# Kernel tuning notes

Measured on AMD Instinct MI355X. Metric: run time of the kernel, lower is better.

The kernel has to match this reference:

```python
import jax, jax.numpy as jnp
import numpy as np

B, N, D, S, ITERS = 64, 4096, 256, 8, 3
EPS = 1e-5


def _ln(x, g, b):
    m = jnp.mean(x, axis=-1, keepdims=True)
    v = jnp.mean((x - m) ** 2, axis=-1, keepdims=True)
    return (x - m) * jax.lax.rsqrt(v + EPS) * g + b


def setup_inputs() -> dict:
    key = jax.random.key(0)
    ks = jax.random.split(key, 20)
    s = 1.0 / np.sqrt(D)
    inp = {
        'x': jax.random.normal(ks[0], (B, N, D), jnp.float32),
        'noise': jax.random.normal(ks[1], (B, S, D), jnp.float32),
        'slot_mu': jax.random.normal(ks[2], (1, 1, D), jnp.float32),
        'slot_sigma': jax.random.normal(ks[3], (1, 1, D), jnp.float32) * 0.1,
        'Wq': jax.random.uniform(ks[4], (D, D), jnp.float32, -s, s),
        'bq': jnp.zeros((D,), jnp.float32),
        'Wk': jax.random.uniform(ks[5], (D, D), jnp.float32, -s, s),
        'bk': jnp.zeros((D,), jnp.float32),
        'Wv': jax.random.uniform(ks[6], (D, D), jnp.float32, -s, s),
        'bv': jnp.zeros((D,), jnp.float32),
        'W_ih': jax.random.uniform(ks[7], (3 * D, D), jnp.float32, -s, s),
        'b_ih': jnp.zeros((3 * D,), jnp.float32),
        'W_hh': jax.random.uniform(ks[8], (3 * D, D), jnp.float32, -s, s),
        'b_hh': jnp.zeros((3 * D,), jnp.float32),
        'W1': jax.random.uniform(ks[9], (D, D), jnp.float32, -s, s),
        'b1': jnp.zeros((D,), jnp.float32),
        'W2': jax.random.uniform(ks[10], (D, D), jnp.float32, -s, s),
        'b2': jnp.zeros((D,), jnp.float32),
        'g_in': jnp.ones((D,), jnp.float32), 'be_in': jnp.zeros((D,), jnp.float32),
        'g_sl': jnp.ones((D,), jnp.float32), 'be_sl': jnp.zeros((D,), jnp.float32),
        'g_mlp': jnp.ones((D,), jnp.float32), 'be_mlp': jnp.zeros((D,), jnp.float32),
    }
    return inp


def reference(x, noise, slot_mu, slot_sigma, Wq, bq, Wk, bk, Wv, bv,
              W_ih, b_ih, W_hh, b_hh, W1, b1, W2, b2,
              g_in, be_in, g_sl, be_sl, g_mlp, be_mlp):
    # slot init: mu + exp(sigma) * noise, broadcast over (B, S, D)
    slots = slot_mu + jnp.exp(slot_sigma) * noise

    xn = _ln(x, g_in, be_in)
    k = jnp.einsum('bnd,ed->bne', xn, Wk) + bk
    v = jnp.einsum('bnd,ed->bne', xn, Wv) + bv

    for _ in range(ITERS):
        sn = _ln(slots, g_sl, be_sl)
        q = jnp.einsum('bsd,ed->bse', sn, Wq) + bq
        attn_logits = jnp.einsum('bsd,bnd->bsn', q, k)
        attn = jax.nn.softmax(attn_logits, axis=-1)  # softmax over inputs N (as in source)
        updates = jnp.einsum('bnd,bsn->bsd', v, attn)

        # GRUCell: input=updates, hidden=slots (flattened over B*S)
        u = updates.reshape(-1, D)
        h = slots.reshape(-1, D)
        gx = u @ W_ih.T + b_ih
        gh = h @ W_hh.T + b_hh
        xr, xz, xn_g = jnp.split(gx, 3, axis=-1)
        hr, hz, hn_g = jnp.split(gh, 3, axis=-1)
        r = jax.nn.sigmoid(xr + hr)
        z = jax.nn.sigmoid(xz + hz)
        n = jnp.tanh(xn_g + r * hn_g)
        h = (1.0 - z) * n + z * h
        slots = h.reshape(x.shape[0], -1, D)

        m = _ln(slots, g_mlp, be_mlp)
        slots = slots + jax.nn.relu(m @ W1.T + b1) @ W2.T + b2
    return slots
```

## Files before the change

kernel.cpp:

```cpp
#include <hip/hip_runtime.h>

#define B_ 64
#define N_ 4096
#define D_ 256
#define S_ 8
#define EPSL 1e-5f

typedef _Float16 f16x8 __attribute__((ext_vector_type(8)));
typedef _Float16 f16x4 __attribute__((ext_vector_type(4)));
typedef float f32x4 __attribute__((ext_vector_type(4)));

__device__ __forceinline__ void gload_lds16(const void* g, void* l){
    __builtin_amdgcn_global_load_lds(
        (const __attribute__((address_space(1))) unsigned int*)g,
        (__attribute__((address_space(3))) unsigned int*)l, 16, 0, 0);
}

__device__ __forceinline__ void a16_st4(_Float16* a, int row, int col, float4 v){
    int byte = row*512 + ((col*2) ^ ((row&7)<<4));
    f16x4 h; h[0]=(_Float16)v.x; h[1]=(_Float16)v.y; h[2]=(_Float16)v.z; h[3]=(_Float16)v.w;
    *(f16x4*)((char*)a + byte) = h;
}
__device__ __forceinline__ void a16_st2(_Float16* a, int row, int col, _Float16 v){
    int byte = row*512 + ((col*2) ^ ((row&7)<<4));
    *(_Float16*)((char*)a + byte) = v;
}
__device__ __forceinline__ f16x8 a16_ld8(const _Float16* a, int row, int col){
    int byte = row*512 + ((col*2) ^ ((row&7)<<4));
    return *(const f16x8*)((const char*)a + byte);
}
__device__ __forceinline__ f16x8 wfrag_ld(const _Float16* __restrict__ Wf,
        int tt, int ks, int l){
    return *(const f16x8*)(Wf + ((long)tt*4096 + (ks*64 + l)*8));
}

__global__ __launch_bounds__(256) void k_ln_x(const float* __restrict__ x,
        const float* __restrict__ g, const float* __restrict__ be,
        _Float16* __restrict__ xn) {
    int w = threadIdx.x >> 6, l = threadIdx.x & 63;
    long row = (long)blockIdx.x * 4 + w;
    float4 xv = *(const float4*)(x + row * D_ + l * 4);
    float s = xv.x + xv.y + xv.z + xv.w;
    float q = xv.x*xv.x + xv.y*xv.y + xv.z*xv.z + xv.w*xv.w;
    #pragma unroll
    for (int m = 1; m < 64; m <<= 1) { s += __shfl_xor(s, m); q += __shfl_xor(q, m); }
    float mean = s * (1.0f/D_);
    float var = q * (1.0f/D_) - mean*mean;
    float inv = rsqrtf(var + EPSL);
    float4 gv = *(const float4*)(g + l*4);
    float4 bv = *(const float4*)(be + l*4);
    f16x4 o;
    o[0] = (_Float16)((xv.x-mean)*inv*gv.x + bv.x);
    o[1] = (_Float16)((xv.y-mean)*inv*gv.y + bv.y);
    o[2] = (_Float16)((xv.z-mean)*inv*gv.z + bv.z);
    o[3] = (_Float16)((xv.w-mean)*inv*gv.w + bv.w);
    *(f16x4*)(xn + row * D_ + l*4) = o;
}

__global__ __launch_bounds__(256) void k_wpre(const float* __restrict__ Whh,
        const float* __restrict__ W1, const float* __restrict__ W2,
        _Float16* __restrict__ Whhf, _Float16* __restrict__ W1f,
        _Float16* __restrict__ W2f,
        const float* __restrict__ Wih, const float* __restrict__ Wv,
        const float* __restrict__ Wq, const float* __restrict__ Wk,
        const float* __restrict__ bih, const float* __restrict__ bv,
        const float* __restrict__ bq, _Float16* __restrict__ Wcf,
        _Float16* __restrict__ Wqkf, float* __restrict__ bc,
        float* __restrict__ cq) {
    __shared__ float a4[4][256];
    int r = blockIdx.x, t = threadIdx.x;
    int w = t>>6, l = t&63;
    if (r >= 256){
        int rr = r - 256;
        const float* src; _Float16* dst; int row;
        if (rr < 768){ src = Whh; dst = Whhf; row = rr; }
        else if (rr < 1024){ src = W1; dst = W1f; row = rr - 768; }
        else { src = W2; dst = W2f; row = rr - 1024; }
        float v = src[(long)row*256 + t];
        long di = (long)((((row>>4)*8 + (t>>5))*64 + ((t>>3)&3)*16 + (row&15)))*8 + (t&7);
        dst[di] = (_Float16)v;
        return;
    }
    bool isC = (r < 192);
    if (isC){
        #pragma unroll
        for (int k=0;k<4;k++) a4[k][t] = Wih[(long)(r*4+k)*256 + t];
    } else {
        int dbase = (r-192)*4;
        #pragma unroll
        for (int k=0;k<4;k++) a4[k][t] = Wk[(long)t*256 + dbase + k];
    }
    __syncthreads();
    float ac[4] = {0.f,0.f,0.f,0.f};
    const float* Bm = isC ? Wv : Wq;
    for (int e=0;e<256;e++){
        float bvv = Bm[(long)e*256 + t];
        ac[0] += a4[0][e]*bvv; ac[1] += a4[1][e]*bvv;
        ac[2] += a4[2][e]*bvv; ac[3] += a4[3][e]*bvv;
    }
    _Float16* dst = isC ? Wcf : Wqkf;
    int rb = isC ? r*4 : (r-192)*4;
    #pragma unroll
    for (int k=0;k<4;k++){
        int row = rb + k;
        long di = (long)((((row>>4)*8 + (t>>5))*64 + ((t>>3)&3)*16 + (row&15)))*8 + (t&7);
        dst[di] = (_Float16)ac[k];
    }
    if (w < 4){
        const float* bvec = isC ? bv : bq;
        float p = 0.f;
        #pragma unroll
        for (int q=0;q<4;q++) p += a4[w][l + q*64] * bvec[l + q*64];
        #pragma unroll
        for (int m=1;m<64;m<<=1) p += __shfl_xor(p, m);
        if (l==0){
            if (isC) bc[r*4 + w] = p + bih[r*4 + w];
            else     cq[(r-192)*4 + w] = p;
        }
    }
}

template<int NT, int OS>
__device__ __forceinline__ void mm_stage_f(const _Float16* a16,
        const _Float16* __restrict__ Wf, float* outl, int w, int l){
    int lr = l&15, lh = l>>4;
    f16x8 A[8];
    #pragma unroll
    for (int ks=0;ks<8;ks++) A[ks] = a16_ld8(a16, lr, lh*8 + ks*32);
    #pragma unroll
    for (int tile=0; tile<NT; ++tile){
        int tt = w*NT + tile;
        f32x4 acc = {0.f,0.f,0.f,0.f};
        #pragma unroll
        for (int ks=0;ks<8;ks++)
            acc = __builtin_amdgcn_mfma_f32_16x16x32_f16(A[ks], wfrag_ld(Wf,tt,ks,l), acc, 0,0,0);
        if (lh < 2){
            #pragma unroll
            for (int r=0;r<4;r++) outl[(lh*4+r)*OS + tt*16 + lr] = acc[r];
        }
    }
}

__device__ __forceinline__ void mm_gates_f(const _Float16* au, const _Float16* ah,
        const _Float16* __restrict__ Wcf, const _Float16* __restrict__ Whf,
        float* g1, float* g2, int w, int l){
    int lr = l&15, lh = l>>4;
    f16x8 Au[8], Ah[8];
    #pragma unroll
    for (int ks=0;ks<8;ks++){ Au[ks] = a16_ld8(au, lr, lh*8+ks*32);
                              Ah[ks] = a16_ld8(ah, lr, lh*8+ks*32); }
    #pragma unroll
    for (int tile=0; tile<6; ++tile){
        int tt = w*6 + tile;
        f32x4 a1 = {0.f,0.f,0.f,0.f}, a2 = {0.f,0.f,0.f,0.f};
        #pragma unroll
        for (int ks=0;ks<8;ks++)
            a1 = __builtin_amdgcn_mfma_f32_16x16x32_f16(Au[ks], wfrag_ld(Wcf,tt,ks,l), a1, 0,0,0);
        #pragma unroll
        for (int ks=0;ks<8;ks++)
            a2 = __builtin_amdgcn_mfma_f32_16x16x32_f16(Ah[ks], wfrag_ld(Whf,tt,ks,l), a2, 0,0,0);
        if (lh < 2){
            #pragma unroll
            for (int r=0;r<4;r++){
                int s = lh*4+r;
                g1[s*768 + tt*16 + lr] = a1[r];
                g2[s*768 + tt*16 + lr] = a2[r];
            }
        }
    }
}

__global__ __launch_bounds__(512) void k_init(const float* __restrict__ noise,
        const float* __restrict__ mu, const float* __restrict__ sg,
        const float* __restrict__ g_sl, const float* __restrict__ be_sl,
        const _Float16* __restrict__ Wqkf, const float* __restrict__ cq,
        float* __restrict__ slots, _Float16* __restrict__ qh16) {
    __shared__ __align__(16) _Float16 a16[16*256];
    __shared__ float g1[8*256];
    int t = threadIdx.x, w = t>>6, l = t&63, b = blockIdx.x;
    int col = l*4;
    float4 nz = *(const float4*)(noise + ((long)b*8+w)*256 + col);
    float4 muv = *(const float4*)(mu + col);
    float4 sgv = *(const float4*)(sg + col);
    float4 sl;
    sl.x = muv.x + __expf(sgv.x)*nz.x; sl.y = muv.y + __expf(sgv.y)*nz.y;
    sl.z = muv.z + __expf(sgv.z)*nz.z; sl.w = muv.w + __expf(sgv.w)*nz.w;
    *(float4*)(slots + ((long)b*8+w)*256 + col) = sl;
    float s1 = sl.x+sl.y+sl.z+sl.w;
    float s2 = sl.x*sl.x+sl.y*sl.y+sl.z*sl.z+sl.w*sl.w;
    #pragma unroll
    for (int m=1;m<64;m<<=1){ s1+=__shfl_xor(s1,m); s2+=__shfl_xor(s2,m); }
    float mean = s1*(1.0f/D_);
    float inv = rsqrtf(s2*(1.0f/D_) - mean*mean + EPSL);
    float4 gv = *(const float4*)(g_sl + col);
    float4 bb = *(const float4*)(be_sl + col);
    float4 sn;
    sn.x=(sl.x-mean)*inv*gv.x+bb.x; sn.y=(sl.y-mean)*inv*gv.y+bb.y;
    sn.z=(sl.z-mean)*inv*gv.z+bb.z; sn.w=(sl.w-mean)*inv*gv.w+bb.w;
    a16_st4(a16, w, col, sn);
    float4 z = {0.f,0.f,0.f,0.f};
    a16_st4(a16, 8+w, col, z);
    __syncthreads();
    mm_stage_f<2,256>(a16, Wqkf, g1, w, l);
    __syncthreads();
    for (int idx=t; idx<2048; idx+=512){
        int s = idx>>8, d = idx&255;
        qh16[((long)b*16+s)*D_ + d] = (_Float16)(g1[s*256+d] + cq[d]);
        qh16[((long)b*16+8+s)*D_ + d] = (_Float16)0.f;
    }
}

__global__ __launch_bounds__(256) void k_attn(const _Float16* __restrict__ xn,
        const _Float16* __restrict__ qh16,
        _Float16* __restrict__ pacc, float* __restrict__ ppsum,
        float* __restrict__ pmax) {
    __shared__ __align__(16) char xt_raw[4*16384];
    __shared__ __align__(16) float pt_s[4][16][8];
    __shared__ float mw_s[4][8], psw_s[4][8];
    int t = threadIdx.x, w = t>>6, l = t&63, lr = l&15, lh = l>>4;
    int c = blockIdx.x, b = blockIdx.y;

    f16x8 A[8];
    const _Float16* qbase = qh16 + ((long)b*16 + lr)*D_ + lh*8;
    #pragma unroll
    for (int ks=0;ks<8;ks++) A[ks] = *(const f16x8*)(qbase + ks*32);
    asm volatile("s_waitcnt vmcnt(0)" ::: "memory");

    char* xw = xt_raw + w*16384;
    const char* xnb = (const char*)(xn + (long)b*N_*D_);
    int rlo = l>>5;
    int cb  = (l&31)*16;

    {   int n0 = c*512 + w*16;
        #pragma unroll
        for (int j=0;j<8;j++){
            int row = 2*j + rlo;
            const char* gp = xnb + (long)(n0+row)*512 + (cb ^ ((row&7)<<4));
            gload_lds16(gp, xw + j*1024);
        }
    }

    float m8[8];
    #pragma unroll
    for (int s=0;s<8;s++) m8[s] = -1e30f;
    float acc[8][4] = {};
    float psr[4] = {0.f,0.f,0.f,0.f};
    float (*pt)[8] = pt_s[w];
    int fx = (lr&7)<<4;

    for (int sc=0; sc<8; ++sc){
        const char* curb = xw + ((sc&1)<<13);
        char* nxtb = xw + (((sc+1)&1)<<13);
        if (sc < 7){
            asm volatile("s_waitcnt lgkmcnt(0)" ::: "memory");
            int n0n = c*512 + (sc+1)*64 + w*16;
            #pragma unroll
            for (int j=0;j<8;j++){
                int row = 2*j + rlo;
                const char* gp = xnb + (long)(n0n+row)*512 + (cb ^ ((row&7)<<4));
                gload_lds16(gp, nxtb + j*1024);
            }
            asm volatile("s_waitcnt vmcnt(8)" ::: "memory");
        } else {
            asm volatile("s_waitcnt vmcnt(0)" ::: "memory");
        }
        __builtin_amdgcn_sched_barrier(0);

        f32x4 lacc = {0.f,0.f,0.f,0.f};
        #pragma unroll
        for (int ks=0;ks<8;ks++){
            f16x8 Bf = *(const f16x8*)(curb + lr*512 + ((lh*16 + ks*64) ^ fx));
            lacc = __builtin_amdgcn_mfma_f32_16x16x32_f16(A[ks], Bf, lacc, 0,0,0);
        }
        float tm[4];
        #pragma unroll
        for (int r=0;r<4;r++) tm[r] = lacc[r];
        #pragma unroll
        for (int m=1;m<16;m<<=1){
            #pragma unroll
            for (int r=0;r<4;r++) tm[r] = fmaxf(tm[r], __shfl_xor(tm[r], m));
        }
        float mN[8];
        #pragma unroll
        for (int r=0;r<4;r++){ mN[r] = __shfl(tm[r], lr); mN[4+r] = __shfl(tm[r], 16+lr); }
        float sc8[8];
        #pragma unroll
        for (int s=0;s<8;s++){
            float mn = fmaxf(m8[s], mN[s]);
            sc8[s] = __expf(m8[s] - mn);
            m8[s] = mn;
        }
        #pragma unroll
        for (int s=0;s<8;s++){
            acc[s][0]*=sc8[s]; acc[s][1]*=sc8[s]; acc[s][2]*=sc8[s]; acc[s][3]*=sc8[s];
        }
        if (lh < 2){
            float4 pv;
            #pragma unroll
            for (int r=0;r<4;r++){
                int s = lh*4+r;
                float p = __expf(lacc[r] - m8[s]);
                psr[r] = psr[r]*sc8[s] + p;
                ((float*)&pv)[r] = p;
            }
            *(float4*)&pt[lr][lh*4] = pv;
        }
        #pragma unroll 4
        for (int i=0;i<16;i++){
            float4 p0 = *(const float4*)&pt[i][0];
            float4 p1 = *(const float4*)&pt[i][4];
            f16x4 xv = *(const f16x4*)(curb + i*512 + ((l*8) ^ ((i&7)<<4)));
            float x0=(float)xv[0], x1=(float)xv[1], x2=(float)xv[2], x3=(float)xv[3];
            acc[0][0]+=p0.x*x0; acc[0][1]+=p0.x*x1; acc[0][2]+=p0.x*x2; acc[0][3]+=p0.x*x3;
            acc[1][0]+=p0.y*x0; acc[1][1]+=p0.y*x1; acc[1][2]+=p0.y*x2; acc[1][3]+=p0.y*x3;
            acc[2][0]+=p0.z*x0; acc[2][1]+=p0.z*x1; acc[2][2]+=p0.z*x2; acc[2][3]+=p0.z*x3;
            acc[3][0]+=p0.w*x0; acc[3][1]+=p0.w*x1; acc[3][2]+=p0.w*x2; acc[3][3]+=p0.w*x3;
            acc[4][0]+=p1.x*x0; acc[4][1]+=p1.x*x1; acc[4][2]+=p1.x*x2; acc[4][3]+=p1.x*x3;
            acc[5][0]+=p1.y*x0; acc[5][1]+=p1.y*x1; acc[5][2]+=p1.y*x2; acc[5][3]+=p1.y*x3;
            acc[6][0]+=p1.z*x0; acc[6][1]+=p1.z*x1; acc[6][2]+=p1.z*x2; acc[6][3]+=p1.z*x3;
            acc[7][0]+=p1.w*x0; acc[7][1]+=p1.w*x1; acc[7][2]+=p1.w*x2; acc[7][3]+=p1.w*x3;
        }
    }
    #pragma unroll
    for (int m=1;m<16;m<<=1){
        #pragma unroll
        for (int r=0;r<4;r++) psr[r] += __shfl_xor(psr[r], m);
    }
    if (l == 0){
        #pragma unroll
        for (int s=0;s<8;s++) mw_s[w][s] = m8[s];
        #pragma unroll
        for (int r=0;r<4;r++) psw_s[w][r] = psr[r];
    }
    if (l == 16){
        #pragma unroll
        for (int r=0;r<4;r++) psw_s[w][4+r] = psr[r];
    }
    __syncthreads();
    float M8[8];
    #pragma unroll
    for (int s=0;s<8;s++)
        M8[s] = fmaxf(fmaxf(mw_s[0][s],mw_s[1][s]), fmaxf(mw_s[2][s],mw_s[3][s]));
    float* accw = (float*)xt_raw;
    #pragma unroll
    for (int s=0;s<8;s++){
        float wsc = __expf(m8[s] - M8[s]);
        float4 v;
        v.x=acc[s][0]*wsc; v.y=acc[s][1]*wsc; v.z=acc[s][2]*wsc; v.w=acc[s][3]*wsc;
        *(float4*)&accw[((w*8+s)<<8) + l*4] = v;
    }
    __syncthreads();
    for (int pair=t; pair<2048; pair+=256){
        int s = pair>>8, d = pair&255;
        float v = accw[(s<<8)+d] + accw[((8+s)<<8)+d] + accw[((16+s)<<8)+d] + accw[((24+s)<<8)+d];
        pacc[(((long)b*8 + c)*8 + s)*D_ + d] = (_Float16)v;
    }
    if (t < 8){
        float ps = 0.f;
        #pragma unroll
        for (int w2=0;w2<4;w2++) ps += __expf(mw_s[w2][t]-M8[t]) * psw_s[w2][t];
        ppsum[((long)b*8+c)*8 + t] = ps;
        pmax [((long)b*8+c)*8 + t] = M8[t];
    }
}

__global__ __launch_bounds__(512) void k_tail(
    const _Float16* __restrict__ pacc, const float* __restrict__ ppsum,
    const float* __restrict__ pmax, const float* __restrict__ slots,
    const _Float16* __restrict__ Wcf, const float* __restrict__ bc,
    const _Float16* __restrict__ Whhf, const float* __restrict__ bhh,
    const _Float16* __restrict__ W1f, const float* __restrict__ b1,
    const _Float16* __restrict__ W2f, const float* __restrict__ b2,
    const float* __restrict__ gm, const float* __restrict__ bem,
    const float* __restrict__ g_sl, const float* __restrict__ be_sl,
    const _Float16* __restrict__ Wqkf, const float* __restrict__ cq,
    float* __restrict__ out, _Float16* __restrict__ qh16, int last) {
    int t = threadIdx.x, w = t>>6, l = t&63;
    int b = blockIdx.x;
    __shared__ float hb[8][256], hn[8][256];
    __shared__ float g1[8*768], g2[8*768];
    __shared__ __align__(16) _Float16 a16a[16*256], a16b[16*256];
    __shared__ float pss[8];
    __shared__ float wcs[8][8];

    if (t < 8){
        float pm[8]; float M = -1e30f;
        #pragma unroll
        for (int c=0;c<8;c++){ pm[c] = pmax[((long)b*8+c)*8+t]; M = fmaxf(M, pm[c]); }
        float ps = 0.f;
        #pragma unroll
        for (int c=0;c<8;c++){
            float wc = __expf(pm[c]-M);
            wcs[t][c] = wc;
            ps += wc*ppsum[((long)b*8+c)*8+t];
        }
        pss[t] = ps;
    }
    __syncthreads();
    for (int idx=t; idx<2048; idx+=512){
        int s = idx>>8, d = idx&255;
        float v = 0.f;
        #pragma unroll
        for (int c=0;c<8;c++) v += wcs[s][c]*(float)pacc[(((long)b*8+c)*8+s)*D_ + d];
        float axv = v / pss[s];
        float hbv = slots[((long)b*8+s)*D_ + d];
        hb[s][d] = hbv;
        a16_st2(a16a, s, d, (_Float16)axv);
        a16_st2(a16b, s, d, (_Float16)hbv);
    }
    {   float4 z = {0.f,0.f,0.f,0.f};
        a16_st4(a16a, 8+w, l*4, z);
        a16_st4(a16b, 8+w, l*4, z);
    }
    __syncthreads();
    mm_gates_f(a16a, a16b, Wcf, Whhf, g1, g2, w, l);
    __syncthreads();
    {
        int d0 = l*4;
        float hn4[4];
        #pragma unroll
        for (int i=0;i<4;i++){
            int d = d0+i;
            float r = 1.f/(1.f+__expf(-(g1[w*768+d]     + bc[d]     + g2[w*768+d]     + bhh[d])));
            float z = 1.f/(1.f+__expf(-(g1[w*768+256+d] + bc[256+d] + g2[w*768+256+d] + bhh[256+d])));
            float gg = g1[w*768+512+d] + bc[512+d] + r*(g2[w*768+512+d] + bhh[512+d]);
            float e2 = __expf(2.f*gg);
            float nn = 1.f - 2.f/(e2+1.f);
            hn4[i] = (1.f-z)*nn + z*hb[w][d];
            hn[w][d] = hn4[i];
        }
        float s1 = hn4[0]+hn4[1]+hn4[2]+hn4[3];
        float s2 = hn4[0]*hn4[0]+hn4[1]*hn4[1]+hn4[2]*hn4[2]+hn4[3]*hn4[3];
        #pragma unroll
        for (int m=1;m<64;m<<=1){ s1+=__shfl_xor(s1,m); s2+=__shfl_xor(s2,m); }
        float mean = s1*(1.0f/D_);
        float inv = rsqrtf(s2*(1.0f/D_) - mean*mean + EPSL);
        float4 gv = *(const float4*)(gm + d0);
        float4 bb = *(const float4*)(bem + d0);
        float4 v;
        v.x=(hn4[0]-mean)*inv*gv.x+bb.x; v.y=(hn4[1]-mean)*inv*gv.y+bb.y;
        v.z=(hn4[2]-mean)*inv*gv.z+bb.z; v.w=(hn4[3]-mean)*inv*gv.w+bb.w;
        a16_st4(a16a, w, d0, v);
    }
    __syncthreads();
    mm_stage_f<2,256>(a16a, W1f, g1, w, l);
    __syncthreads();
    {
        int d0 = l*4;
        float4 v = *(const float4*)&g1[w*256+d0];
        float4 bb = *(const float4*)(b1 + d0);
        v.x=fmaxf(v.x+bb.x,0.f); v.y=fmaxf(v.y+bb.y,0.f);
        v.z=fmaxf(v.z+bb.z,0.f); v.w=fmaxf(v.w+bb.w,0.f);
        a16_st4(a16b, w, d0, v);
    }
    __syncthreads();
    mm_stage_f<2,256>(a16b, W2f, g2, w, l);
    __syncthreads();
    {
        int d0 = l*4;
        float4 bb = *(const float4*)(b2 + d0);
        float4 o4;
        o4.x = hn[w][d0]   + g2[w*256+d0]   + bb.x;
        o4.y = hn[w][d0+1] + g2[w*256+d0+1] + bb.y;
        o4.z = hn[w][d0+2] + g2[w*256+d0+2] + bb.z;
        o4.w = hn[w][d0+3] + g2[w*256+d0+3] + bb.w;
        *(float4*)(out + ((long)b*8+w)*D_ + d0) = o4;
        if (!last){
            float s1 = o4.x+o4.y+o4.z+o4.w;
            float s2 = o4.x*o4.x+o4.y*o4.y+o4.z*o4.z+o4.w*o4.w;
            #pragma unroll
            for (int m=1;m<64;m<<=1){ s1+=__shfl_xor(s1,m); s2+=__shfl_xor(s2,m); }
            float mean = s1*(1.0f/D_);
            float inv = rsqrtf(s2*(1.0f/D_) - mean*mean + EPSL);
            float4 gv = *(const float4*)(g_sl + d0);
            float4 be = *(const float4*)(be_sl + d0);
            float4 v;
            v.x=(o4.x-mean)*inv*gv.x+be.x; v.y=(o4.y-mean)*inv*gv.y+be.y;
            v.z=(o4.z-mean)*inv*gv.z+be.z; v.w=(o4.w-mean)*inv*gv.w+be.w;
            a16_st4(a16a, w, d0, v);
        }
    }
    if (last) return;
    __syncthreads();
    mm_stage_f<2,256>(a16a, Wqkf, g1, w, l);
    __syncthreads();
    for (int idx=t; idx<2048; idx+=512){
        int s = idx>>8, d = idx&255;
        qh16[((long)b*16+s)*D_ + d] = (_Float16)(g1[s*256+d] + cq[d]);
    }
}

extern "C" void kernel_launch(void* const* d_in, const int* in_sizes, int n_in,
                              void* d_out, int out_size, void* d_ws, size_t ws_size,
                              hipStream_t stream) {
    const float* x     = (const float*)d_in[0];
    const float* noise = (const float*)d_in[1];
    const float* mu    = (const float*)d_in[2];
    const float* sg    = (const float*)d_in[3];
    const float* Wq    = (const float*)d_in[4];
    const float* bq    = (const float*)d_in[5];
    const float* Wk    = (const float*)d_in[6];
    const float* Wv    = (const float*)d_in[8];
    const float* bv    = (const float*)d_in[9];
    const float* Wih   = (const float*)d_in[10];
    const float* bih   = (const float*)d_in[11];
    const float* Whh   = (const float*)d_in[12];
    const float* bhh   = (const float*)d_in[13];
    const float* W1    = (const float*)d_in[14];
    const float* b1    = (const float*)d_in[15];
    const float* W2    = (const float*)d_in[16];
    const float* b2    = (const float*)d_in[17];
    const float* g_in  = (const float*)d_in[18];
    const float* be_in = (const float*)d_in[19];
    const float* g_sl  = (const float*)d_in[20];
    const float* be_sl = (const float*)d_in[21];
    const float* g_mlp = (const float*)d_in[22];
    const float* be_mlp= (const float*)d_in[23];

    char* ws = (char*)d_ws;
    _Float16* xn16  = (_Float16*)(ws);
    _Float16* qh16  = (_Float16*)(ws + 134217728);
    float*    slots = (float*)   (ws + 134742016);
    _Float16* pacc  = (_Float16*)(ws + 135266304);
    float*    ppsum = (float*)   (ws + 152043520);
    float*    pmax  = (float*)   (ws + 152059904);
    _Float16* w16f  = (_Float16*)(ws + 152076288);
    float*    bc    = (float*)   (ws + 153255936);
    float*    cq    = (float*)   (ws + 153259008);

    _Float16* Wcf  = w16f;
    _Float16* Whhf = w16f + 196608;
    _Float16* W1f  = w16f + 393216;
    _Float16* W2f  = w16f + 458752;
    _Float16* Wqkf = w16f + 524288;

    hipLaunchKernelGGL(k_wpre, dim3(1536), dim3(256), 0, stream,
                       Whh, W1, W2, Whhf, W1f, W2f,
                       Wih, Wv, Wq, Wk, bih, bv, bq, Wcf, Wqkf, bc, cq);
    hipLaunchKernelGGL(k_ln_x, dim3(65536), dim3(256), 0, stream, x, g_in, be_in, xn16);
    hipLaunchKernelGGL(k_init, dim3(64), dim3(512), 0, stream,
                       noise, mu, sg, g_sl, be_sl, Wqkf, cq, slots, qh16);
    for (int it = 0; it < 3; it++){
        hipLaunchKernelGGL(k_attn, dim3(8,64), dim3(256), 0, stream,
                           xn16, qh16, pacc, ppsum, pmax);
        float* dst = (it==2) ? (float*)d_out : slots;
        hipLaunchKernelGGL(k_tail, dim3(64), dim3(512), 0, stream,
                           pacc, ppsum, pmax, slots,
                           Wcf, bc, Whhf, bhh, W1f, b1, W2f, b2,
                           g_mlp, be_mlp, g_sl, be_sl, Wqkf, cq,
                           dst, qh16, (it==2) ? 1 : 0);
    }
}
```

Before: 269.0 us.

## Fuse input LayerNorm into first attention pass and use nontemporal LDS loads

Removes the standalone LayerNorm kernel over x and computes the normalization inside a new first-iteration attention kernel. That kernel normalizes fp32 rows, writes the fp16 result to LDS for immediate use, and also stores it to global memory for later iterations. This avoids one full write-then-read pass of the normalized activations in the first iteration. The fused kernel loses the async double-buffered prefetch and exposes register-heavy fp32 loads. The later attention kernels now use a nontemporal cache hint on their global-to-LDS loads.

```diff
diff --git a/kernel.cpp b/kernel.cpp
--- a/kernel.cpp
+++ b/kernel.cpp
@@ -10,10 +10,10 @@
 typedef _Float16 f16x4 __attribute__((ext_vector_type(4)));
 typedef float f32x4 __attribute__((ext_vector_type(4)));
 
-__device__ __forceinline__ void gload_lds16(const void* g, void* l){
+__device__ __forceinline__ void gload_lds16_nt(const void* g, void* l){
     __builtin_amdgcn_global_load_lds(
         (const __attribute__((address_space(1))) unsigned int*)g,
-        (__attribute__((address_space(3))) unsigned int*)l, 16, 0, 0);
+        (__attribute__((address_space(3))) unsigned int*)l, 16, 0, 2);
 }
 
 __device__ __forceinline__ void a16_st4(_Float16* a, int row, int col, float4 v){
@@ -32,29 +32,6 @@
 __device__ __forceinline__ f16x8 wfrag_ld(const _Float16* __restrict__ Wf,
         int tt, int ks, int l){
     return *(const f16x8*)(Wf + ((long)tt*4096 + (ks*64 + l)*8));
-}
-
-__global__ __launch_bounds__(256) void k_ln_x(const float* __restrict__ x,
-        const float* __restrict__ g, const float* __restrict__ be,
-        _Float16* __restrict__ xn) {
-    int w = threadIdx.x >> 6, l = threadIdx.x & 63;
-    long row = (long)blockIdx.x * 4 + w;
-    float4 xv = *(const float4*)(x + row * D_ + l * 4);
-    float s = xv.x + xv.y + xv.z + xv.w;
-    float q = xv.x*xv.x + xv.y*xv.y + xv.z*xv.z + xv.w*xv.w;
-    #pragma unroll
-    for (int m = 1; m < 64; m <<= 1) { s += __shfl_xor(s, m); q += __shfl_xor(q, m); }
-    float mean = s * (1.0f/D_);
-    float var = q * (1.0f/D_) - mean*mean;
-    float inv = rsqrtf(var + EPSL);
-    float4 gv = *(const float4*)(g + l*4);
-    float4 bv = *(const float4*)(be + l*4);
-    f16x4 o;
-    o[0] = (_Float16)((xv.x-mean)*inv*gv.x + bv.x);
-    o[1] = (_Float16)((xv.y-mean)*inv*gv.y + bv.y);
-    o[2] = (_Float16)((xv.z-mean)*inv*gv.z + bv.z);
-    o[3] = (_Float16)((xv.w-mean)*inv*gv.w + bv.w);
-    *(f16x4*)(xn + row * D_ + l*4) = o;
 }
 
 __global__ __launch_bounds__(256) void k_wpre(const float* __restrict__ Whh,
@@ -210,6 +187,170 @@
     }
 }
 
+__global__ __launch_bounds__(256) void k_attn1(const float* __restrict__ x,
+        const float* __restrict__ g_in, const float* __restrict__ be_in,
+        _Float16* __restrict__ xn,
+        const _Float16* __restrict__ qh16,
+        _Float16* __restrict__ pacc, float* __restrict__ ppsum,
+        float* __restrict__ pmax) {
+    __shared__ __align__(16) char xt_raw[4*16384];
+    __shared__ __align__(16) float pt_s[4][16][8];
+    __shared__ float mw_s[4][8], psw_s[4][8];
+    int t = threadIdx.x, w = t>>6, l = t&63, lr = l&15, lh = l>>4;
+    int c = blockIdx.x, b = blockIdx.y;
+
+    f16x8 A[8];
+    const _Float16* qbase = qh16 + ((long)b*16 + lr)*D_ + lh*8;
+    #pragma unroll
+    for (int ks=0;ks<8;ks++) A[ks] = *(const f16x8*)(qbase + ks*32);
+
+    char* xw = xt_raw + w*16384;
+    int rq = l>>2, q = l&3;
+
+    float m8[8];
+    #pragma unroll
+    for (int s=0;s<8;s++) m8[s] = -1e30f;
+    float acc[8][4] = {};
+    float psr[4] = {0.f,0.f,0.f,0.f};
+    float (*pt)[8] = pt_s[w];
+    int fx = (lr&7)<<4;
+
+    for (int sc=0; sc<8; ++sc){
+        char* curb = xw + ((sc&1)<<13);
+        int n0 = c*512 + sc*64 + w*16;
+        const float* xf = x + ((long)(b*N_) + n0 + rq)*D_ + q*64;
+        float4 xv[16];
+        #pragma unroll
+        for (int i=0;i<16;i++) xv[i] = *(const float4*)(xf + i*4);
+        float s1 = 0.f, s2 = 0.f;
+        #pragma unroll
+        for (int i=0;i<16;i++){
+            s1 += xv[i].x + xv[i].y + xv[i].z + xv[i].w;
+            s2 += xv[i].x*xv[i].x + xv[i].y*xv[i].y + xv[i].z*xv[i].z + xv[i].w*xv[i].w;
+        }
+        s1 += __shfl_xor(s1, 1); s2 += __shfl_xor(s2, 1);
+        s1 += __shfl_xor(s1, 2); s2 += __shfl_xor(s2, 2);
+        float mean = s1 * (1.0f/D_);
+        float inv = rsqrtf(s2 * (1.0f/D_) - mean*mean + EPSL);
+        int swz = (rq&7)<<4;
+        _Float16* gout = xn + ((long)(b*N_) + n0 + rq)*D_ + q*64;
+        #pragma unroll
+        for (int k=0;k<8;k++){
+            float4 v0 = xv[k*2], v1 = xv[k*2+1];
+            float4 gv0 = *(const float4*)(g_in + q*64 + k*8);
+            float4 gv1 = *(const float4*)(g_in + q*64 + k*8 + 4);
+            float4 bb0 = *(const float4*)(be_in + q*64 + k*8);
+            float4 bb1 = *(const float4*)(be_in + q*64 + k*8 + 4);
+            f16x8 o;
+            o[0]=(_Float16)((v0.x-mean)*inv*gv0.x+bb0.x);
+            o[1]=(_Float16)((v0.y-mean)*inv*gv0.y+bb0.y);
+            o[2]=(_Float16)((v0.z-mean)*inv*gv0.z+bb0.z);
+            o[3]=(_Float16)((v0.w-mean)*inv*gv0.w+bb0.w);
+            o[4]=(_Float16)((v1.x-mean)*inv*gv1.x+bb1.x);
+            o[5]=(_Float16)((v1.y-mean)*inv*gv1.y+bb1.y);
+            o[6]=(_Float16)((v1.z-mean)*inv*gv1.z+bb1.z);
+            o[7]=(_Float16)((v1.w-mean)*inv*gv1.w+bb1.w);
+            *(f16x8*)(curb + rq*512 + ((q*128 + k*16) ^ swz)) = o;
+            *(f16x8*)(gout + k*8) = o;
+        }
+        f32x4 lacc = {0.f,0.f,0.f,0.f};
+        #pragma unroll
+        for (int ks=0;ks<8;ks++){
+            f16x8 Bf = *(const f16x8*)(curb + lr*512 + ((lh*16 + ks*64) ^ fx));
+            lacc = __builtin_amdgcn_mfma_f32_16x16x32_f16(A[ks], Bf, lacc, 0,0,0);
+        }
+        float tm[4];
+        #pragma unroll
+        for (int r=0;r<4;r++) tm[r] = lacc[r];
+        #pragma unroll
+        for (int m=1;m<16;m<<=1){
+            #pragma unroll
+            for (int r=0;r<4;r++) tm[r] = fmaxf(tm[r], __shfl_xor(tm[r], m));
+        }
+        float mN[8];
+        #pragma unroll
+        for (int r=0;r<4;r++){ mN[r] = __shfl(tm[r], lr); mN[4+r] = __shfl(tm[r], 16+lr); }
+        float sc8[8];
+        #pragma unroll
+        for (int s=0;s<8;s++){
+            float mn = fmaxf(m8[s], mN[s]);
+            sc8[s] = __expf(m8[s] - mn);
+            m8[s] = mn;
+        }
+        #pragma unroll
+        for (int s=0;s<8;s++){
+            acc[s][0]*=sc8[s]; acc[s][1]*=sc8[s]; acc[s][2]*=sc8[s]; acc[s][3]*=sc8[s];
+        }
+        if (lh < 2){
+            float4 pv;
+            #pragma unroll
+            for (int r=0;r<4;r++){
+                int s = lh*4+r;
+                float p = __expf(lacc[r] - m8[s]);
+                psr[r] = psr[r]*sc8[s] + p;
+                ((float*)&pv)[r] = p;
+            }
+            *(float4*)&pt[lr][lh*4] = pv;
+        }
+        #pragma unroll 4
+        for (int i=0;i<16;i++){
+            float4 p0 = *(const float4*)&pt[i][0];
+            float4 p1 = *(const float4*)&pt[i][4];
+            f16x4 xvv = *(const f16x4*)(curb + i*512 + ((l*8) ^ ((i&7)<<4)));
+            float x0=(float)xvv[0], x1=(float)xvv[1], x2=(float)xvv[2], x3=(float)xvv[3];
+            acc[0][0]+=p0.x*x0; acc[0][1]+=p0.x*x1; acc[0][2]+=p0.x*x2; acc[0][3]+=p0.x*x3;
+            acc[1][0]+=p0.y*x0; acc[1][1]+=p0.y*x1; acc[1][2]+=p0.y*x2; acc[1][3]+=p0.y*x3;
+            acc[2][0]+=p0.z*x0; acc[2][1]+=p0.z*x1; acc[2][2]+=p0.z*x2; acc[2][3]+=p0.z*x3;
+            acc[3][0]+=p0.w*x0; acc[3][1]+=p0.w*x1; acc[3][2]+=p0.w*x2; acc[3][3]+=p0.w*x3;
+            acc[4][0]+=p1.x*x0; acc[4][1]+=p1.x*x1; acc[4][2]+=p1.x*x2; acc[4][3]+=p1.x*x3;
+            acc[5][0]+=p1.y*x0; acc[5][1]+=p1.y*x1; acc[5][2]+=p1.y*x2; acc[5][3]+=p1.y*x3;
+            acc[6][0]+=p1.z*x0; acc[6][1]+=p1.z*x1; acc[6][2]+=p1.z*x2; acc[6][3]+=p1.z*x3;
+            acc[7][0]+=p1.w*x0; acc[7][1]+=p1.w*x1; acc[7][2]+=p1.w*x2; acc[7][3]+=p1.w*x3;
+        }
+    }
+    #pragma unroll
+    for (int m=1;m<16;m<<=1){
+        #pragma unroll
+        for (int r=0;r<4;r++) psr[r] += __shfl_xor(psr[r], m);
+    }
+    if (l == 0){
+        #pragma unroll
+        for (int s=0;s<8;s++) mw_s[w][s] = m8[s];
+        #pragma unroll
+        for (int r=0;r<4;r++) psw_s[w][r] = psr[r];
+    }
+    if (l == 16){
+        #pragma unroll
+        for (int r=0;r<4;r++) psw_s[w][4+r] = psr[r];
+    }
+    __syncthreads();
+    float M8[8];
+    #pragma unroll
+    for (int s=0;s<8;s++)
+        M8[s] = fmaxf(fmaxf(mw_s[0][s],mw_s[1][s]), fmaxf(mw_s[2][s],mw_s[3][s]));
+    float* accw = (float*)xt_raw;
+    #pragma unroll
+    for (int s=0;s<8;s++){
+        float wsc = __expf(m8[s] - M8[s]);
+        float4 v;
+        v.x=acc[s][0]*wsc; v.y=acc[s][1]*wsc; v.z=acc[s][2]*wsc; v.w=acc[s][3]*wsc;
+        *(float4*)&accw[((w*8+s)<<8) + l*4] = v;
+    }
+    __syncthreads();
+    for (int pair=t; pair<2048; pair+=256){
+        int s = pair>>8, d = pair&255;
+        float v = accw[(s<<8)+d] + accw[((8+s)<<8)+d] + accw[((16+s)<<8)+d] + accw[((24+s)<<8)+d];
+        pacc[(((long)b*8 + c)*8 + s)*D_ + d] = (_Float16)v;
+    }
+    if (t < 8){
+        float ps = 0.f;
+        #pragma unroll
+        for (int w2=0;w2<4;w2++) ps += __expf(mw_s[w2][t]-M8[t]) * psw_s[w2][t];
+        ppsum[((long)b*8+c)*8 + t] = ps;
+        pmax [((long)b*8+c)*8 + t] = M8[t];
+    }
+}
+
 __global__ __launch_bounds__(256) void k_attn(const _Float16* __restrict__ xn,
         const _Float16* __restrict__ qh16,
         _Float16* __restrict__ pacc, float* __restrict__ ppsum,
@@ -236,7 +377,7 @@
         for (int j=0;j<8;j++){
             int row = 2*j + rlo;
             const char* gp = xnb + (long)(n0+row)*512 + (cb ^ ((row&7)<<4));
-            gload_lds16(gp, xw + j*1024);
+            gload_lds16_nt(gp, xw + j*1024);
         }
     }
 
@@ -258,7 +399,7 @@
             for (int j=0;j<8;j++){
                 int row = 2*j + rlo;
                 const char* gp = xnb + (long)(n0n+row)*512 + (cb ^ ((row&7)<<4));
-                gload_lds16(gp, nxtb + j*1024);
+                gload_lds16_nt(gp, nxtb + j*1024);
             }
             asm volatile("s_waitcnt vmcnt(8)" ::: "memory");
         } else {
@@ -537,12 +678,15 @@
     hipLaunchKernelGGL(k_wpre, dim3(1536), dim3(256), 0, stream,
                        Whh, W1, W2, Whhf, W1f, W2f,
                        Wih, Wv, Wq, Wk, bih, bv, bq, Wcf, Wqkf, bc, cq);
-    hipLaunchKernelGGL(k_ln_x, dim3(65536), dim3(256), 0, stream, x, g_in, be_in, xn16);
     hipLaunchKernelGGL(k_init, dim3(64), dim3(512), 0, stream,
                        noise, mu, sg, g_sl, be_sl, Wqkf, cq, slots, qh16);
     for (int it = 0; it < 3; it++){
-        hipLaunchKernelGGL(k_attn, dim3(8,64), dim3(256), 0, stream,
-                           xn16, qh16, pacc, ppsum, pmax);
+        if (it == 0)
+            hipLaunchKernelGGL(k_attn1, dim3(8,64), dim3(256), 0, stream,
+                               x, g_in, be_in, xn16, qh16, pacc, ppsum, pmax);
+        else
+            hipLaunchKernelGGL(k_attn, dim3(8,64), dim3(256), 0, stream,
+                               xn16, qh16, pacc, ppsum, pmax);
         float* dst = (it==2) ? (float*)d_out : slots;
         hipLaunchKernelGGL(k_tail, dim3(64), dim3(512), 0, stream,
                            pacc, ppsum, pmax, slots,
```

Measured after the change: 281.7 us. +4.7%, slower.

## Single-buffer attention tiles with non-temporal loads and widen LN-x rows

Applied to the files above, without the earlier changes.

The attention kernel goes from double-buffered LDS tiles to a single 8KB buffer per wave. The next tile's load is now issued after the current tile's compute finishes, which halves LDS use so more blocks can fit per CU, at the cost of losing load/compute overlap within a wave. Tile loads now use a non-temporal cache hint. The input LayerNorm kernel processes two rows per wave with 8-element vectors and launches half as many blocks.

```diff
diff --git a/kernel.cpp b/kernel.cpp
--- a/kernel.cpp
+++ b/kernel.cpp
@@ -10,10 +10,10 @@
 typedef _Float16 f16x4 __attribute__((ext_vector_type(4)));
 typedef float f32x4 __attribute__((ext_vector_type(4)));
 
-__device__ __forceinline__ void gload_lds16(const void* g, void* l){
+__device__ __forceinline__ void gload_lds16_nt(const void* g, void* l){
     __builtin_amdgcn_global_load_lds(
         (const __attribute__((address_space(1))) unsigned int*)g,
-        (__attribute__((address_space(3))) unsigned int*)l, 16, 0, 0);
+        (__attribute__((address_space(3))) unsigned int*)l, 16, 0, 2);
 }
 
 __device__ __forceinline__ void a16_st4(_Float16* a, int row, int col, float4 v){
@@ -38,23 +38,31 @@
         const float* __restrict__ g, const float* __restrict__ be,
         _Float16* __restrict__ xn) {
     int w = threadIdx.x >> 6, l = threadIdx.x & 63;
-    long row = (long)blockIdx.x * 4 + w;
-    float4 xv = *(const float4*)(x + row * D_ + l * 4);
-    float s = xv.x + xv.y + xv.z + xv.w;
-    float q = xv.x*xv.x + xv.y*xv.y + xv.z*xv.z + xv.w*xv.w;
-    #pragma unroll
-    for (int m = 1; m < 64; m <<= 1) { s += __shfl_xor(s, m); q += __shfl_xor(q, m); }
+    int half = l >> 5, li = l & 31;
+    long row = (long)blockIdx.x * 8 + w*2 + half;
+    const float* xr = x + row * D_ + li * 8;
+    float4 a = *(const float4*)(xr);
+    float4 b = *(const float4*)(xr + 4);
+    float s = a.x+a.y+a.z+a.w + b.x+b.y+b.z+b.w;
+    float q = a.x*a.x+a.y*a.y+a.z*a.z+a.w*a.w + b.x*b.x+b.y*b.y+b.z*b.z+b.w*b.w;
+    #pragma unroll
+    for (int m = 1; m < 32; m <<= 1) { s += __shfl_xor(s, m); q += __shfl_xor(q, m); }
     float mean = s * (1.0f/D_);
-    float var = q * (1.0f/D_) - mean*mean;
-    float inv = rsqrtf(var + EPSL);
-    float4 gv = *(const float4*)(g + l*4);
-    float4 bv = *(const float4*)(be + l*4);
-    f16x4 o;
-    o[0] = (_Float16)((xv.x-mean)*inv*gv.x + bv.x);
-    o[1] = (_Float16)((xv.y-mean)*inv*gv.y + bv.y);
-    o[2] = (_Float16)((xv.z-mean)*inv*gv.z + bv.z);
-    o[3] = (_Float16)((xv.w-mean)*inv*gv.w + bv.w);
-    *(f16x4*)(xn + row * D_ + l*4) = o;
+    float inv = rsqrtf(q * (1.0f/D_) - mean*mean + EPSL);
+    float4 gv0 = *(const float4*)(g + li*8);
+    float4 gv1 = *(const float4*)(g + li*8 + 4);
+    float4 bb0 = *(const float4*)(be + li*8);
+    float4 bb1 = *(const float4*)(be + li*8 + 4);
+    f16x8 o;
+    o[0]=(_Float16)((a.x-mean)*inv*gv0.x+bb0.x);
+    o[1]=(_Float16)((a.y-mean)*inv*gv0.y+bb0.y);
+    o[2]=(_Float16)((a.z-mean)*inv*gv0.z+bb0.z);
+    o[3]=(_Float16)((a.w-mean)*inv*gv0.w+bb0.w);
+    o[4]=(_Float16)((b.x-mean)*inv*gv1.x+bb1.x);
+    o[5]=(_Float16)((b.y-mean)*inv*gv1.y+bb1.y);
+    o[6]=(_Float16)((b.z-mean)*inv*gv1.z+bb1.z);
+    o[7]=(_Float16)((b.w-mean)*inv*gv1.w+bb1.w);
+    *(f16x8*)(xn + row * D_ + li*8) = o;
 }
 
 __global__ __launch_bounds__(256) void k_wpre(const float* __restrict__ Whh,
@@ -214,7 +222,7 @@
         const _Float16* __restrict__ qh16,
         _Float16* __restrict__ pacc, float* __restrict__ ppsum,
         float* __restrict__ pmax) {
-    __shared__ __align__(16) char xt_raw[4*16384];
+    __shared__ __align__(16) char xt_raw[4*8192];
     __shared__ __align__(16) float pt_s[4][16][8];
     __shared__ float mw_s[4][8], psw_s[4][8];
     int t = threadIdx.x, w = t>>6, l = t&63, lr = l&15, lh = l>>4;
@@ -226,7 +234,7 @@
     for (int ks=0;ks<8;ks++) A[ks] = *(const f16x8*)(qbase + ks*32);
     asm volatile("s_waitcnt vmcnt(0)" ::: "memory");
 
-    char* xw = xt_raw + w*16384;
+    char* xw = xt_raw + w*8192;
     const char* xnb = (const char*)(xn + (long)b*N_*D_);
     int rlo = l>>5;
     int cb  = (l&31)*16;
@@ -236,7 +244,7 @@
         for (int j=0;j<8;j++){
             int row = 2*j + rlo;
             const char* gp = xnb + (long)(n0+row)*512 + (cb ^ ((row&7)<<4));
-            gload_lds16(gp, xw + j*1024);
+            gload_lds16_nt(gp, xw + j*1024);
         }
     }
 
@@ -249,27 +257,13 @@
     int fx = (lr&7)<<4;
 
     for (int sc=0; sc<8; ++sc){
-        const char* curb = xw + ((sc&1)<<13);
-        char* nxtb = xw + (((sc+1)&1)<<13);
-        if (sc < 7){
-            asm volatile("s_waitcnt lgkmcnt(0)" ::: "memory");
-            int n0n = c*512 + (sc+1)*64 + w*16;
-            #pragma unroll
-            for (int j=0;j<8;j++){
-                int row = 2*j + rlo;
-                const char* gp = xnb + (long)(n0n+row)*512 + (cb ^ ((row&7)<<4));
-                gload_lds16(gp, nxtb + j*1024);
-            }
-            asm volatile("s_waitcnt vmcnt(8)" ::: "memory");
-        } else {
-            asm volatile("s_waitcnt vmcnt(0)" ::: "memory");
-        }
+        asm volatile("s_waitcnt vmcnt(0)" ::: "memory");
         __builtin_amdgcn_sched_barrier(0);
 
         f32x4 lacc = {0.f,0.f,0.f,0.f};
         #pragma unroll
         for (int ks=0;ks<8;ks++){
-            f16x8 Bf = *(const f16x8*)(curb + lr*512 + ((lh*16 + ks*64) ^ fx));
+            f16x8 Bf = *(const f16x8*)(xw + lr*512 + ((lh*16 + ks*64) ^ fx));
             lacc = __builtin_amdgcn_mfma_f32_16x16x32_f16(A[ks], Bf, lacc, 0,0,0);
         }
         float tm[4];
@@ -309,7 +303,7 @@
         for (int i=0;i<16;i++){
             float4 p0 = *(const float4*)&pt[i][0];
             float4 p1 = *(const float4*)&pt[i][4];
-            f16x4 xv = *(const f16x4*)(curb + i*512 + ((l*8) ^ ((i&7)<<4)));
+            f16x4 xv = *(const f16x4*)(xw + i*512 + ((l*8) ^ ((i&7)<<4)));
             float x0=(float)xv[0], x1=(float)xv[1], x2=(float)xv[2], x3=(float)xv[3];
             acc[0][0]+=p0.x*x0; acc[0][1]+=p0.x*x1; acc[0][2]+=p0.x*x2; acc[0][3]+=p0.x*x3;
             acc[1][0]+=p0.y*x0; acc[1][1]+=p0.y*x1; acc[1][2]+=p0.y*x2; acc[1][3]+=p0.y*x3;
@@ -319,6 +313,17 @@
             acc[5][0]+=p1.y*x0; acc[5][1]+=p1.y*x1; acc[5][2]+=p1.y*x2; acc[5][3]+=p1.y*x3;
             acc[6][0]+=p1.z*x0; acc[6][1]+=p1.z*x1; acc[6][2]+=p1.z*x2; acc[6][3]+=p1.z*x3;
             acc[7][0]+=p1.w*x0; acc[7][1]+=p1.w*x1; acc[7][2]+=p1.w*x2; acc[7][3]+=p1.w*x3;
+        }
+        if (sc < 7){
+            asm volatile("s_waitcnt lgkmcnt(0)" ::: "memory");
+            __builtin_amdgcn_sched_barrier(0);
+            int n0n = c*512 + (sc+1)*64 + w*16;
+            #pragma unroll
+            for (int j=0;j<8;j++){
+                int row = 2*j + rlo;
+                const char* gp = xnb + (long)(n0n+row)*512 + (cb ^ ((row&7)<<4));
+                gload_lds16_nt(gp, xw + j*1024);
+            }
         }
     }
     #pragma unroll
@@ -537,7 +542,7 @@
     hipLaunchKernelGGL(k_wpre, dim3(1536), dim3(256), 0, stream,
                        Whh, W1, W2, Whhf, W1f, W2f,
                        Wih, Wv, Wq, Wk, bih, bv, bq, Wcf, Wqkf, bc, cq);
-    hipLaunchKernelGGL(k_ln_x, dim3(65536), dim3(256), 0, stream, x, g_in, be_in, xn16);
+    hipLaunchKernelGGL(k_ln_x, dim3(32768), dim3(256), 0, stream, x, g_in, be_in, xn16);
     hipLaunchKernelGGL(k_init, dim3(64), dim3(512), 0, stream,
                        noise, mu, sg, g_sl, be_sl, Wqkf, cq, slots, qh16);
     for (int it = 0; it < 3; it++){
```

Result: faster. 255.6 us (-5.0%).
